# Kernel optimization log

Measured on AMD Instinct MI355X. Metric: run time of the kernel, lower is better.

## Reference

```python
import jax, jax.numpy as jnp
import numpy as np

B, T, D, H, FF_MULT, WINDOW = 4, 2048, 256, 8, 4, 64
HD = D // H
FF = FF_MULT * D
EPS = 1e-5


def _layer_norm(x, g, b):
    m = jnp.mean(x, axis=-1, keepdims=True)
    v = jnp.mean(jnp.square(x - m), axis=-1, keepdims=True)
    return (x - m) / jnp.sqrt(v + EPS) * g + b


def setup_inputs() -> dict:
    key = jax.random.key(0)
    ks = jax.random.split(key, 6)
    scale = 0.02
    return {
        "x": jax.random.normal(ks[0], (B, T, D), jnp.float32),
        "ln1_g": jnp.ones((D,), jnp.float32),
        "ln1_b": jnp.zeros((D,), jnp.float32),
        "in_proj_w": jax.random.normal(ks[1], (D, 3 * D), jnp.float32) * scale,
        "in_proj_b": jnp.zeros((3 * D,), jnp.float32),
        "out_w": jax.random.normal(ks[2], (D, D), jnp.float32) * scale,
        "out_b": jnp.zeros((D,), jnp.float32),
        "ln2_g": jnp.ones((D,), jnp.float32),
        "ln2_b": jnp.zeros((D,), jnp.float32),
        "w1": jax.random.normal(ks[3], (D, FF), jnp.float32) * scale,
        "b1": jnp.zeros((FF,), jnp.float32),
        "w2": jax.random.normal(ks[4], (FF, D), jnp.float32) * scale,
        "b2": jnp.zeros((D,), jnp.float32),
        "window": WINDOW,
    }


def reference(x, ln1_g, ln1_b, in_proj_w, in_proj_b, out_w, out_b,
              ln2_g, ln2_b, w1, b1, w2, b2, window):
    Bv, Tv, Dv = x.shape
    xn = _layer_norm(x, ln1_g, ln1_b)                      # norm1(x) used as q,k,v
    qkv = xn @ in_proj_w + in_proj_b                       # [B,T,3D]
    q, k, v = jnp.split(qkv, 3, axis=-1)

    def to_heads(t):
        return t.reshape(Bv, Tv, H, HD).transpose(0, 2, 1, 3)  # [B,H,T,HD]

    q, k, v = to_heads(q), to_heads(k), to_heads(v)
    scores = jnp.einsum('bhqd,bhkd->bhqk', q, k) / jnp.sqrt(jnp.float32(HD))
    i = jnp.arange(Tv)[:, None]
    j = jnp.arange(Tv)[None, :]
    band = jnp.abs(j - i) <= window                        # True = allowed
    scores = jnp.where(band, scores, -jnp.inf)
    attn = jax.nn.softmax(scores, axis=-1)
    o = jnp.einsum('bhqk,bhkd->bhqd', attn, v)
    o = o.transpose(0, 2, 1, 3).reshape(Bv, Tv, Dv)
    h_out = o @ out_w + out_b                              # attn output
    y = x + h_out
    ff = _layer_norm(y, ln2_g, ln2_b)
    ff = jax.nn.gelu(ff @ w1 + b1, approximate=False) @ w2 + b2
    return x + ff                                          # note: residual from x, not y
```

## Files before the change

kernel.cpp:

```cpp
#include <hip/hip_runtime.h>
#include <math.h>

#define T_SEQ 2048

typedef float  fx4 __attribute__((ext_vector_type(4)));
typedef short  sx4 __attribute__((ext_vector_type(4)));
typedef short  sx8 __attribute__((ext_vector_type(8)));
typedef unsigned short u16;

static __device__ __forceinline__ u16 f2b(float f) {
  unsigned u = __builtin_bit_cast(unsigned, f);
  u += 0x7fffu + ((u >> 16) & 1u);
  return (u16)(u >> 16);
}
static __device__ __forceinline__ float b2f(u16 v) {
  unsigned u = ((unsigned)v) << 16;
  return __builtin_bit_cast(float, u);
}

static __device__ __forceinline__ fx4 mfma16(sx4 a, sx4 b, fx4 c) {
  return __builtin_amdgcn_mfma_f32_16x16x16bf16_1k(a, b, c, 0, 0, 0);
}
static __device__ __forceinline__ fx4 mfma32(sx8 a, sx8 b, fx4 c) {
  return __builtin_amdgcn_mfma_f32_16x16x32_bf16(a, b, c, 0, 0, 0);
}

static __device__ __forceinline__ void gload16(const void* g, void* l) {
  __builtin_amdgcn_global_load_lds(
      (const __attribute__((address_space(1))) unsigned*)g,
      (__attribute__((address_space(3))) unsigned*)l, 16, 0, 0);
}

__global__ __launch_bounds__(256) void prep_k(
    const float* __restrict__ x, const float* __restrict__ g1,
    const float* __restrict__ b1, u16* __restrict__ xn, u16* __restrict__ xb,
    const float* __restrict__ ipw, const float* __restrict__ outw,
    const float* __restrict__ w1, const float* __restrict__ w2,
    u16* __restrict__ ipwT, u16* __restrict__ outwT,
    u16* __restrict__ w1T, u16* __restrict__ w2T) {
  const int bid = blockIdx.x;
  if (bid < 2048) {
    const int row = bid * 4 + (threadIdx.x >> 6);
    const int l = threadIdx.x & 63;
    fx4 v = *(const fx4*)&x[(size_t)row * 256 + l * 4];
    float s = v.x + v.y + v.z + v.w;
    float q = v.x * v.x + v.y * v.y + v.z * v.z + v.w * v.w;
#pragma unroll
    for (int off = 1; off < 64; off <<= 1) {
      s += __shfl_xor(s, off);
      q += __shfl_xor(q, off);
    }
    const float mean = s * (1.0f / 256.0f);
    const float var = q * (1.0f / 256.0f) - mean * mean;
    const float rstd = rsqrtf(var + 1e-5f);
    fx4 gv = *(const fx4*)&g1[l * 4];
    fx4 bv = *(const fx4*)&b1[l * 4];
    sx4 o, xo;
    o[0] = (short)f2b((v.x - mean) * rstd * gv.x + bv.x);
    o[1] = (short)f2b((v.y - mean) * rstd * gv.y + bv.y);
    o[2] = (short)f2b((v.z - mean) * rstd * gv.z + bv.z);
    o[3] = (short)f2b((v.w - mean) * rstd * gv.w + bv.w);
    xo[0] = (short)f2b(v.x);
    xo[1] = (short)f2b(v.y);
    xo[2] = (short)f2b(v.z);
    xo[3] = (short)f2b(v.w);
    *(sx4*)&xn[(size_t)row * 256 + l * 4] = o;
    *(sx4*)&xb[(size_t)row * 256 + l * 4] = xo;
    return;
  }
  const int tb = bid - 2048;
  const float* in; u16* out; int K, N, loc;
  if (tb < 192)      { in = ipw;  out = ipwT;  K = 256;  N = 768;  loc = tb; }
  else if (tb < 256) { in = outw; out = outwT; K = 256;  N = 256;  loc = tb - 192; }
  else if (tb < 512) { in = w1;   out = w1T;   K = 256;  N = 1024; loc = tb - 256; }
  else               { in = w2;   out = w2T;   K = 1024; N = 256;  loc = tb - 512; }
  const int ntx = N >> 5;
  const int by = (loc / ntx) << 5;
  const int bx = (loc % ntx) << 5;
  __shared__ float t[32][33];
  const int c = threadIdx.x & 31, r0 = threadIdx.x >> 5;
#pragma unroll
  for (int i = 0; i < 4; ++i)
    t[r0 + i * 8][c] = in[(size_t)(by + r0 + i * 8) * N + bx + c];
  __syncthreads();
#pragma unroll
  for (int i = 0; i < 4; ++i) {
    const int r = r0 + i * 8;
    out[(size_t)(bx + r) * K + by + c] = f2b(t[c][r]);
  }
}

template <int BM, int BN, int KD, int ND, int OP, int NGRP>
__global__ __launch_bounds__(256) void gemm3_k(const u16* __restrict__ A,
                                               const u16* __restrict__ Wt,
                                               const float* __restrict__ bias,
                                               const float* __restrict__ resid,
                                               void* __restrict__ outp) {
  constexpr int BK = 64;
  constexpr int WM = BM / 2, WN = BN / 2;
  constexpr int FM = WM / 16, FN = WN / 16;
  constexpr int NT = KD / BK;
  __shared__ __align__(16) char smem[(2 * BM + 2 * BN) * BK * 2];
  auto As = (u16(*)[BM][BK])smem;
  auto Bs = (u16(*)[BN][BK])(smem + 2 * BM * BK * 2);
  const int tid = threadIdx.x;
  const int id = blockIdx.x;
  const int bm = ((id & 7) + 8 * ((id >> 3) / NGRP)) * BM;
  const int bn = ((id >> 3) % NGRP) * BN;
  const int l = tid & 63, wid = tid >> 6;
  const int wm = wid >> 1, wn = wid & 1;
  const int lq = l & 15, lg = l >> 4;

  auto stage = [&](int buf, int k0) {
#pragma unroll
    for (int i = 0; i < (BM * BK) / 2048; ++i) {
      const int row = (tid >> 3) + 32 * i;
      const int c = (tid & 7) ^ (row & 7);
      gload16(&A[(size_t)(bm + row) * KD + k0 + c * 8], &As[buf][row][(tid & 7) * 8]);
    }
#pragma unroll
    for (int i = 0; i < (BN * BK) / 2048; ++i) {
      const int row = (tid >> 3) + 32 * i;
      const int c = (tid & 7) ^ (row & 7);
      gload16(&Wt[(size_t)(bn + row) * KD + k0 + c * 8], &Bs[buf][row][(tid & 7) * 8]);
    }
  };

  fx4 acc[FM][FN] = {};
  stage(0, 0);
  int cur = 0;
  for (int t = 0; t < NT; ++t) {
    __syncthreads();
    if (t + 1 < NT) stage(cur ^ 1, (t + 1) * BK);
#pragma unroll
    for (int kk = 0; kk < BK; kk += 32) {
      sx8 aF[FM], bF[FN];
#pragma unroll
      for (int m = 0; m < FM; ++m) {
        const int row = wm * WM + m * 16 + lq;
        const int c = ((kk >> 3) + lg) ^ (row & 7);
        aF[m] = *(const sx8*)&As[cur][row][c * 8];
      }
#pragma unroll
      for (int n = 0; n < FN; ++n) {
        const int row = wn * WN + n * 16 + lq;
        const int c = ((kk >> 3) + lg) ^ (row & 7);
        bF[n] = *(const sx8*)&Bs[cur][row][c * 8];
      }
#pragma unroll
      for (int m = 0; m < FM; ++m)
#pragma unroll
        for (int n = 0; n < FN; ++n) acc[m][n] = mfma32(aF[m], bF[n], acc[m][n]);
    }
    cur ^= 1;
  }

  __syncthreads();
  if (OP == 1) {
    auto C = (float(*)[BN + 8])smem;
#pragma unroll
    for (int m = 0; m < FM; ++m)
#pragma unroll
      for (int n = 0; n < FN; ++n) {
        const int col = wn * WN + n * 16 + lq;
        const float bv = bias[bn + col];
#pragma unroll
        for (int r = 0; r < 4; ++r)
          C[wm * WM + m * 16 + lg * 4 + r][col] = acc[m][n][r] + bv;
      }
    __syncthreads();
    constexpr int CH = (BM * BN / 4) / 256;
#pragma unroll
    for (int i = 0; i < CH; ++i) {
      const int t = tid + i * 256;
      const int row = t / (BN / 4), c = t % (BN / 4);
      fx4 v = *(const fx4*)&C[row][c * 4];
      const fx4 rr = *(const fx4*)&resid[(size_t)(bm + row) * ND + bn + c * 4];
      v += rr;
      *(fx4*)&((float*)outp)[(size_t)(bm + row) * ND + bn + c * 4] = v;
    }
  } else {
    auto C = (u16(*)[BN + 8])smem;
#pragma unroll
    for (int m = 0; m < FM; ++m)
#pragma unroll
      for (int n = 0; n < FN; ++n) {
        const int col = wn * WN + n * 16 + lq;
        const float bv = bias[bn + col];
#pragma unroll
        for (int r = 0; r < 4; ++r) {
          float v = acc[m][n][r] + bv;
          if (OP == 2) v = 0.5f * v * (1.0f + erff(v * 0.70710678118654752f));
          C[wm * WM + m * 16 + lg * 4 + r][col] = f2b(v);
        }
      }
    __syncthreads();
    constexpr int CH = (BM * BN / 8) / 256;
#pragma unroll
    for (int i = 0; i < CH; ++i) {
      const int t = tid + i * 256;
      const int row = t / (BN / 8), c = t % (BN / 8);
      *(sx8*)&((u16*)outp)[(size_t)(bm + row) * ND + bn + c * 8] = *(const sx8*)&C[row][c * 8];
    }
  }
}

__global__ __launch_bounds__(256) void gemmln_k(const u16* __restrict__ A,
                                                const u16* __restrict__ Wt,
                                                const float* __restrict__ bias,
                                                const u16* __restrict__ xb,
                                                const float* __restrict__ g,
                                                const float* __restrict__ bv2,
                                                u16* __restrict__ yn) {
  __shared__ __align__(16) char smem[18944];
  auto As = (u16(*)[32])smem;
  auto Bs = (u16(*)[32])(smem + 2048);
  auto red = (float(*)[2][2])(smem + 18432);
  auto Ys = (u16(*)[264])smem;
  const int tid = threadIdx.x;
  const int bm = blockIdx.x * 32;
  const int l = tid & 63, wid = tid >> 6;
  const int wm = wid >> 1, wn = wid & 1;
  const int lq = l & 15, lg = l >> 4;
  const int sr = tid >> 2, sc = (tid & 3) << 3;
  fx4 acc[8] = {};
  for (int k0 = 0; k0 < 256; k0 += 32) {
    if (tid < 128) gload16(&A[(size_t)(bm + (tid >> 2)) * 256 + k0 + ((tid & 3) << 3)],
                           &As[tid >> 2][(tid & 3) << 3]);
#pragma unroll
    for (int i = 0; i < 4; ++i)
      gload16(&Wt[(size_t)(sr + i * 64) * 256 + k0 + sc], &Bs[sr + i * 64][sc]);
    __syncthreads();
    const sx8 aF = *(const sx8*)&As[wm * 16 + lq][8 * lg];
#pragma unroll
    for (int n = 0; n < 8; ++n) {
      const sx8 bF = *(const sx8*)&Bs[wn * 128 + n * 16 + lq][8 * lg];
      acc[n] = mfma32(aF, bF, acc[n]);
    }
    __syncthreads();
  }
  float vv[8][4];
  float s[4] = {}, q[4] = {};
#pragma unroll
  for (int n = 0; n < 8; ++n) {
    const int col = wn * 128 + n * 16 + lq;
    const float bb = bias[col];
#pragma unroll
    for (int r = 0; r < 4; ++r) {
      const int row = bm + wm * 16 + lg * 4 + r;
      const float v = acc[n][r] + bb + b2f(xb[(size_t)row * 256 + col]);
      vv[n][r] = v;
      s[r] += v;
      q[r] += v * v;
    }
  }
#pragma unroll
  for (int off = 1; off < 16; off <<= 1) {
#pragma unroll
    for (int r = 0; r < 4; ++r) {
      s[r] += __shfl_xor(s[r], off);
      q[r] += __shfl_xor(q[r], off);
    }
  }
  if (lq == 0) {
#pragma unroll
    for (int r = 0; r < 4; ++r) {
      red[wm * 16 + lg * 4 + r][wn][0] = s[r];
      red[wm * 16 + lg * 4 + r][wn][1] = q[r];
    }
  }
  __syncthreads();
  float mean4[4], rs4[4];
#pragma unroll
  for (int r = 0; r < 4; ++r) {
    const int rr = wm * 16 + lg * 4 + r;
    const float st = red[rr][0][0] + red[rr][1][0];
    const float qt = red[rr][0][1] + red[rr][1][1];
    mean4[r] = st * (1.0f / 256.0f);
    const float var = qt * (1.0f / 256.0f) - mean4[r] * mean4[r];
    rs4[r] = rsqrtf(var + 1e-5f);
  }
  __syncthreads();
#pragma unroll
  for (int n = 0; n < 8; ++n) {
    const int col = wn * 128 + n * 16 + lq;
    const float gc = g[col], bc = bv2[col];
#pragma unroll
    for (int r = 0; r < 4; ++r)
      Ys[wm * 16 + lg * 4 + r][col] = f2b((vv[n][r] - mean4[r]) * rs4[r] * gc + bc);
  }
  __syncthreads();
#pragma unroll
  for (int i = 0; i < 4; ++i) {
    const int t = tid + i * 256;
    const int row = t >> 5, c = t & 31;
    *(sx8*)&yn[(size_t)(bm + row) * 256 + c * 8] = *(const sx8*)&Ys[row][c * 8];
  }
}

__global__ __launch_bounds__(512) void attn_k(const u16* __restrict__ qkv,
                                              u16* __restrict__ o) {
  __shared__ u16 Qs[128][32];
  __shared__ u16 Ks[256][32];
  __shared__ u16 Vs[32][264];
  const int blk = blockIdx.x;
  const int tile = blk & 15;
  const int bh = blk >> 4;
  const int h = bh & 7;
  const int b = bh >> 3;
  const int q0 = tile << 7;
  const int kstart = max(0, q0 - 64);
  const int kend = min(T_SEQ, q0 + 192);
  const int nk = kend - kstart;
  const int tid = threadIdx.x;
  const float scale = 0.17677669529663687f;

  {
    const int r = tid >> 2, c8 = (tid & 3) << 3;
    gload16(&qkv[(size_t)(b * T_SEQ + q0 + r) * 768 + h * 32 + c8], &Qs[r][c8]);
  }
  for (int r0 = 0; r0 < nk; r0 += 128) {
    const int r = r0 + (tid >> 2);
    if (r < nk) {
      const int c8 = (tid & 3) << 3;
      gload16(&qkv[(size_t)(b * T_SEQ + kstart + r) * 768 + 256 + h * 32 + c8], &Ks[r][c8]);
    }
  }
  for (int e = tid * 4; e < nk * 32; e += 2048) {
    const int r = e >> 5, c = e & 31;
    sx4 v = *(const sx4*)&qkv[(size_t)(b * T_SEQ + kstart + r) * 768 + 512 + h * 32 + c];
    Vs[c + 0][r] = v[0];
    Vs[c + 1][r] = v[1];
    Vs[c + 2][r] = v[2];
    Vs[c + 3][r] = v[3];
  }
  __syncthreads();

  const int w = tid >> 6, l = tid & 63;
  const int lq = l & 15, lg = l >> 4;
  const int qw0 = q0 + w * 16;
  const int iq = qw0 + lq;
  const sx8 qB = *(const sx8*)&Qs[w * 16 + lq][8 * lg];
  float lsum = 0.0f;
  fx4 acc0 = {0.f, 0.f, 0.f, 0.f}, acc1 = {0.f, 0.f, 0.f, 0.f};
  const int rt0 = max(0, qw0 - 64 - kstart) >> 4;
  const int rt1 = (min(kend, qw0 + 80) - kstart) >> 4;
  for (int rt = rt0; rt < rt1; ++rt) {
    const int kb = kstart + (rt << 4);
    const sx8 kA = *(const sx8*)&Ks[(rt << 4) + lq][8 * lg];
    fx4 zero = {0.f, 0.f, 0.f, 0.f};
    fx4 sc = mfma32(kA, qB, zero);
    sx4 pB;
#pragma unroll
    for (int r = 0; r < 4; ++r) {
      const int dd = kb + 4 * lg + r - iq;
      const float sv = (dd >= -64 && dd <= 64) ? fminf(sc[r] * scale, 30.0f) : -100.0f;
      const float p = __expf(sv);
      lsum += p;
      pB[r] = (short)f2b(p);
    }
    const sx4 vA0 = *(const sx4*)&Vs[lq][(rt << 4) + 4 * lg];
    const sx4 vA1 = *(const sx4*)&Vs[16 + lq][(rt << 4) + 4 * lg];
    acc0 = mfma16(vA0, pB, acc0);
    acc1 = mfma16(vA1, pB, acc1);
  }
  lsum += __shfl_xor(lsum, 16);
  lsum += __shfl_xor(lsum, 32);
  const float rl = 1.0f / lsum;

  __syncthreads();
  auto Os = (u16(*)[32])Qs;
#pragma unroll
  for (int r = 0; r < 4; ++r) {
    Os[w * 16 + lq][4 * lg + r] = f2b(acc0[r] * rl);
    Os[w * 16 + lq][16 + 4 * lg + r] = f2b(acc1[r] * rl);
  }
  __syncthreads();
  {
    const int row = tid >> 2, c = tid & 3;
    *(sx8*)&o[(size_t)(b * T_SEQ + q0 + row) * 256 + h * 32 + c * 8] =
        *(const sx8*)&Os[row][c * 8];
  }
}

extern "C" void kernel_launch(void* const* d_in, const int* in_sizes, int n_in,
                              void* d_out, int out_size, void* d_ws, size_t ws_size,
                              hipStream_t stream) {
  const float* x    = (const float*)d_in[0];
  const float* ln1g = (const float*)d_in[1];
  const float* ln1b = (const float*)d_in[2];
  const float* ipw  = (const float*)d_in[3];
  const float* ipb  = (const float*)d_in[4];
  const float* outw = (const float*)d_in[5];
  const float* outb = (const float*)d_in[6];
  const float* ln2g = (const float*)d_in[7];
  const float* ln2b = (const float*)d_in[8];
  const float* w1   = (const float*)d_in[9];
  const float* b1   = (const float*)d_in[10];
  const float* w2   = (const float*)d_in[11];
  const float* b2   = (const float*)d_in[12];

  char* ws = (char*)d_ws;
  u16*   xn   = (u16*)(ws);
  u16*   qkvb = (u16*)(ws + (4ull << 20));
  u16*   o    = (u16*)(ws + (16ull << 20));
  u16*   yn   = (u16*)(ws + (20ull << 20));
  u16*   hh   = (u16*)(ws + (24ull << 20));
  u16*   xb   = (u16*)(ws + (40ull << 20));
  u16*   ipwT = (u16*)(ws + (44ull << 20));
  u16*   outwT= (u16*)(ws + (44ull << 20) + (512ull << 10));
  u16*   w1T  = (u16*)(ws + (45ull << 20));
  u16*   w2T  = (u16*)(ws + (45ull << 20) + (512ull << 10));

  prep_k<<<2816, 256, 0, stream>>>(x, ln1g, ln1b, xn, xb, ipw, outw, w1, w2,
                                   ipwT, outwT, w1T, w2T);
  gemm3_k<128, 128, 256, 768, 0, 6><<<384, 256, 0, stream>>>(xn, ipwT, ipb, nullptr, qkvb);
  attn_k<<<512, 512, 0, stream>>>(qkvb, o);
  gemmln_k<<<256, 256, 0, stream>>>(o, outwT, outb, xb, ln2g, ln2b, yn);
  gemm3_k<128, 128, 256, 1024, 2, 8><<<512, 256, 0, stream>>>(yn, w1T, b1, nullptr, hh);
  gemm3_k<64, 128, 1024, 256, 1, 2><<<256, 256, 0, stream>>>(hh, w2T, b2, x, (float*)d_out);
}
```

Baseline: 62.68 us.

## Fuse both MLP GEMMs and GELU into one kernel keeping hidden in LDS

Replaces the two MLP GEMM launches (FC1+GELU writing the hidden activation to global memory, then FC2+residual) with a single kernel. Each block owns 32 rows, loops over 64-wide hidden chunks, computes FC1+GELU into shared memory and accumulates FC2 directly, double-buffering the weight chunks. This removes the global round trip of the 8192x1024 hidden tensor and one launch. In exchange it uses only 256 blocks with about 148KB of shared memory each (one block per CU), adds more barriers per chunk, and every block re-reads all of W1 and W2.

Result: slower. 70.54 us (+12.5%).

```diff
diff --git a/kernel.cpp b/kernel.cpp
--- a/kernel.cpp
+++ b/kernel.cpp
@@ -156,8 +156,8 @@
   }
 
   __syncthreads();
-  if (OP == 1) {
-    auto C = (float(*)[BN + 8])smem;
+  {
+    auto C = (u16(*)[BN + 8])smem;
 #pragma unroll
     for (int m = 0; m < FM; ++m)
 #pragma unroll
@@ -165,32 +165,8 @@
         const int col = wn * WN + n * 16 + lq;
         const float bv = bias[bn + col];
 #pragma unroll
-        for (int r = 0; r < 4; ++r)
-          C[wm * WM + m * 16 + lg * 4 + r][col] = acc[m][n][r] + bv;
-      }
-    __syncthreads();
-    constexpr int CH = (BM * BN / 4) / 256;
-#pragma unroll
-    for (int i = 0; i < CH; ++i) {
-      const int t = tid + i * 256;
-      const int row = t / (BN / 4), c = t % (BN / 4);
-      fx4 v = *(const fx4*)&C[row][c * 4];
-      const fx4 rr = *(const fx4*)&resid[(size_t)(bm + row) * ND + bn + c * 4];
-      v += rr;
-      *(fx4*)&((float*)outp)[(size_t)(bm + row) * ND + bn + c * 4] = v;
-    }
-  } else {
-    auto C = (u16(*)[BN + 8])smem;
-#pragma unroll
-    for (int m = 0; m < FM; ++m)
-#pragma unroll
-      for (int n = 0; n < FN; ++n) {
-        const int col = wn * WN + n * 16 + lq;
-        const float bv = bias[bn + col];
-#pragma unroll
         for (int r = 0; r < 4; ++r) {
           float v = acc[m][n][r] + bv;
-          if (OP == 2) v = 0.5f * v * (1.0f + erff(v * 0.70710678118654752f));
           C[wm * WM + m * 16 + lg * 4 + r][col] = f2b(v);
         }
       }
@@ -383,6 +359,124 @@
   }
 }
 
+__global__ __launch_bounds__(256) void mlp_k(const u16* __restrict__ yn,
+                                             const u16* __restrict__ w1T,
+                                             const u16* __restrict__ w2T,
+                                             const float* __restrict__ b1,
+                                             const float* __restrict__ b2,
+                                             const float* __restrict__ x,
+                                             float* __restrict__ out) {
+  __shared__ __align__(16) char smem[151552];
+  auto As = (u16(*)[32][64])smem;
+  auto Hs = (u16(*)[64])(smem + 16384);
+  const int tid = threadIdx.x;
+  const int bm = blockIdx.x * 32;
+  const int l = tid & 63, wid = tid >> 6;
+  const int lq = l & 15, lg = l >> 4;
+
+#pragma unroll
+  for (int s = 0; s < 4; ++s) {
+    const int row = tid >> 3, ch = tid & 7;
+    gload16(&yn[(size_t)(bm + row) * 256 + s * 64 + ((ch ^ (row & 7)) << 3)],
+            &As[s][row][ch << 3]);
+  }
+  auto stage_w = [&](int b, int c) {
+    auto W1 = (u16(*)[64][64])(smem + 20480 + b * 32768);
+    auto W2 = (u16(*)[64])(smem + 86016 + b * 32768);
+#pragma unroll
+    for (int j = 0; j < 8; ++j) {
+      const int p = tid + j * 256;
+      const int s = p >> 9, w = p & 511, row = w >> 3, ch = w & 7;
+      gload16(&w1T[(size_t)(c * 64 + row) * 256 + s * 64 + ((ch ^ (row & 7)) << 3)],
+              &W1[s][row][ch << 3]);
+    }
+#pragma unroll
+    for (int j = 0; j < 8; ++j) {
+      const int p = tid + j * 256;
+      const int row = p >> 3, ch = p & 7;
+      gload16(&w2T[(size_t)row * 1024 + c * 64 + ((ch ^ (row & 7)) << 3)],
+              &W2[row][ch << 3]);
+    }
+  };
+
+  fx4 acc[2][4] = {};
+  stage_w(0, 0);
+  __syncthreads();
+  int cur = 0;
+  for (int c = 0; c < 16; ++c) {
+    if (c) __syncthreads();
+    if (c + 1 < 16) stage_w(cur ^ 1, c + 1);
+    auto W1 = (u16(*)[64][64])(smem + 20480 + cur * 32768);
+    auto W2 = (u16(*)[64])(smem + 86016 + cur * 32768);
+    const int rfw = wid * 16 + lq;
+    fx4 hacc0 = {0.f, 0.f, 0.f, 0.f}, hacc1 = {0.f, 0.f, 0.f, 0.f};
+#pragma unroll
+    for (int s = 0; s < 4; ++s)
+#pragma unroll
+      for (int kk = 0; kk < 2; ++kk) {
+        const int cc = kk * 4 + lg;
+        const sx8 bF = *(const sx8*)&W1[s][rfw][(cc ^ (rfw & 7)) << 3];
+        const sx8 aF0 = *(const sx8*)&As[s][lq][(cc ^ (lq & 7)) << 3];
+        const sx8 aF1 = *(const sx8*)&As[s][16 + lq][(cc ^ (lq & 7)) << 3];
+        hacc0 = mfma32(aF0, bF, hacc0);
+        hacc1 = mfma32(aF1, bF, hacc1);
+      }
+    const float bb1 = b1[c * 64 + rfw];
+#pragma unroll
+    for (int r = 0; r < 4; ++r) {
+      {
+        float v = hacc0[r] + bb1;
+        v = 0.5f * v * (1.0f + erff(v * 0.70710678118654752f));
+        const int row = 4 * lg + r;
+        Hs[row][(((rfw >> 3) ^ (row & 7)) << 3) | (rfw & 7)] = f2b(v);
+      }
+      {
+        float v = hacc1[r] + bb1;
+        v = 0.5f * v * (1.0f + erff(v * 0.70710678118654752f));
+        const int row = 16 + 4 * lg + r;
+        Hs[row][(((rfw >> 3) ^ (row & 7)) << 3) | (rfw & 7)] = f2b(v);
+      }
+    }
+    asm volatile("s_waitcnt lgkmcnt(0)\n\ts_barrier" ::: "memory");
+#pragma unroll
+    for (int kk = 0; kk < 2; ++kk) {
+      const int cc = kk * 4 + lg;
+      const sx8 aH0 = *(const sx8*)&Hs[lq][(cc ^ (lq & 7)) << 3];
+      const sx8 aH1 = *(const sx8*)&Hs[16 + lq][(cc ^ (lq & 7)) << 3];
+#pragma unroll
+      for (int n = 0; n < 4; ++n) {
+        const int rw = wid * 64 + n * 16 + lq;
+        const sx8 bW = *(const sx8*)&W2[rw][(cc ^ (rw & 7)) << 3];
+        acc[0][n] = mfma32(aH0, bW, acc[0][n]);
+        acc[1][n] = mfma32(aH1, bW, acc[1][n]);
+      }
+    }
+    cur ^= 1;
+  }
+
+  __syncthreads();
+  auto Cs = (float(*)[264])smem;
+#pragma unroll
+  for (int n = 0; n < 4; ++n) {
+    const int col = wid * 64 + n * 16 + lq;
+    const float bb = b2[col];
+#pragma unroll
+    for (int m = 0; m < 2; ++m)
+#pragma unroll
+      for (int r = 0; r < 4; ++r)
+        Cs[m * 16 + 4 * lg + r][col] = acc[m][n][r] + bb;
+  }
+  __syncthreads();
+#pragma unroll
+  for (int j = 0; j < 8; ++j) {
+    const int p = tid + j * 256;
+    const int row = p >> 6, c4 = (p & 63) << 2;
+    fx4 v = *(const fx4*)&Cs[row][c4];
+    v += *(const fx4*)&x[(size_t)(bm + row) * 256 + c4];
+    *(fx4*)&out[(size_t)(bm + row) * 256 + c4] = v;
+  }
+}
+
 extern "C" void kernel_launch(void* const* d_in, const int* in_sizes, int n_in,
                               void* d_out, int out_size, void* d_ws, size_t ws_size,
                               hipStream_t stream) {
@@ -405,18 +499,16 @@
   u16*   qkvb = (u16*)(ws + (4ull << 20));
   u16*   o    = (u16*)(ws + (16ull << 20));
   u16*   yn   = (u16*)(ws + (20ull << 20));
-  u16*   hh   = (u16*)(ws + (24ull << 20));
-  u16*   xb   = (u16*)(ws + (40ull << 20));
-  u16*   ipwT = (u16*)(ws + (44ull << 20));
-  u16*   outwT= (u16*)(ws + (44ull << 20) + (512ull << 10));
-  u16*   w1T  = (u16*)(ws + (45ull << 20));
-  u16*   w2T  = (u16*)(ws + (45ull << 20) + (512ull << 10));
+  u16*   xb   = (u16*)(ws + (24ull << 20));
+  u16*   ipwT = (u16*)(ws + (28ull << 20));
+  u16*   outwT= (u16*)(ws + (28ull << 20) + (512ull << 10));
+  u16*   w1T  = (u16*)(ws + (29ull << 20));
+  u16*   w2T  = (u16*)(ws + (29ull << 20) + (512ull << 10));
 
   prep_k<<<2816, 256, 0, stream>>>(x, ln1g, ln1b, xn, xb, ipw, outw, w1, w2,
                                    ipwT, outwT, w1T, w2T);
   gemm3_k<128, 128, 256, 768, 0, 6><<<384, 256, 0, stream>>>(xn, ipwT, ipb, nullptr, qkvb);
   attn_k<<<512, 512, 0, stream>>>(qkvb, o);
   gemmln_k<<<256, 256, 0, stream>>>(o, outwT, outb, xb, ln2g, ln2b, yn);
-  gemm3_k<128, 128, 256, 1024, 2, 8><<<512, 256, 0, stream>>>(yn, w1T, b1, nullptr, hh);
-  gemm3_k<64, 128, 1024, 256, 1, 2><<<256, 256, 0, stream>>>(hh, w2T, b2, x, (float*)d_out);
-}
+  mlp_k<<<256, 256, 0, stream>>>(yn, w1T, w2T, b1, b2, x, (float*)d_out);
+}
```

## Use 8-wave blocks for GEMMs and double-buffer the out-proj+LN GEMM

Applied to the files above, without the earlier changes.

Doubles the threads per block in all GEMM kernels from 256 to 512, arranging waves in a 2x4 grid so each wave owns a smaller output tile. This adds latency hiding per block and shrinks per-wave accumulator registers. The out-projection plus LayerNorm kernel is reworked to use 64-wide K steps with double-buffered swizzled LDS staging, replacing its single-buffered loop with two barriers per step. In exchange it uses much more shared memory per block (about 73 KB), which may limit how many blocks fit on a CU, and it gives each wave fewer MFMAs per LDS load.

After: 59.15 us. 1.06x faster.

```diff
diff --git a/kernel.cpp b/kernel.cpp
--- a/kernel.cpp
+++ b/kernel.cpp
@@ -91,14 +91,14 @@
 }
 
 template <int BM, int BN, int KD, int ND, int OP, int NGRP>
-__global__ __launch_bounds__(256) void gemm3_k(const u16* __restrict__ A,
+__global__ __launch_bounds__(512) void gemm5_k(const u16* __restrict__ A,
                                                const u16* __restrict__ Wt,
                                                const float* __restrict__ bias,
                                                const float* __restrict__ resid,
                                                void* __restrict__ outp) {
   constexpr int BK = 64;
-  constexpr int WM = BM / 2, WN = BN / 2;
-  constexpr int FM = WM / 16, FN = WN / 16;
+  constexpr int WTM = BM / 2, WTN = BN / 4;
+  constexpr int FM = WTM / 16, FN = WTN / 16;
   constexpr int NT = KD / BK;
   __shared__ __align__(16) char smem[(2 * BM + 2 * BN) * BK * 2];
   auto As = (u16(*)[BM][BK])smem;
@@ -108,21 +108,23 @@
   const int bm = ((id & 7) + 8 * ((id >> 3) / NGRP)) * BM;
   const int bn = ((id >> 3) % NGRP) * BN;
   const int l = tid & 63, wid = tid >> 6;
-  const int wm = wid >> 1, wn = wid & 1;
+  const int wr = wid >> 2, wc = wid & 3;
   const int lq = l & 15, lg = l >> 4;
 
   auto stage = [&](int buf, int k0) {
 #pragma unroll
-    for (int i = 0; i < (BM * BK) / 2048; ++i) {
-      const int row = (tid >> 3) + 32 * i;
-      const int c = (tid & 7) ^ (row & 7);
-      gload16(&A[(size_t)(bm + row) * KD + k0 + c * 8], &As[buf][row][(tid & 7) * 8]);
-    }
-#pragma unroll
-    for (int i = 0; i < (BN * BK) / 2048; ++i) {
-      const int row = (tid >> 3) + 32 * i;
-      const int c = (tid & 7) ^ (row & 7);
-      gload16(&Wt[(size_t)(bn + row) * KD + k0 + c * 8], &Bs[buf][row][(tid & 7) * 8]);
+    for (int i = 0; i < BM / 64; ++i) {
+      const int p = tid + i * 512;
+      const int row = p >> 3, ch = p & 7;
+      gload16(&A[(size_t)(bm + row) * KD + k0 + ((ch ^ (row & 7)) << 3)],
+              &As[buf][row][ch << 3]);
+    }
+#pragma unroll
+    for (int i = 0; i < BN / 64; ++i) {
+      const int p = tid + i * 512;
+      const int row = p >> 3, ch = p & 7;
+      gload16(&Wt[(size_t)(bn + row) * KD + k0 + ((ch ^ (row & 7)) << 3)],
+              &Bs[buf][row][ch << 3]);
     }
   };
 
@@ -137,15 +139,13 @@
       sx8 aF[FM], bF[FN];
 #pragma unroll
       for (int m = 0; m < FM; ++m) {
-        const int row = wm * WM + m * 16 + lq;
-        const int c = ((kk >> 3) + lg) ^ (row & 7);
-        aF[m] = *(const sx8*)&As[cur][row][c * 8];
+        const int row = wr * WTM + m * 16 + lq;
+        aF[m] = *(const sx8*)&As[cur][row][((((kk >> 3) + lg) ^ (row & 7)) << 3)];
       }
 #pragma unroll
       for (int n = 0; n < FN; ++n) {
-        const int row = wn * WN + n * 16 + lq;
-        const int c = ((kk >> 3) + lg) ^ (row & 7);
-        bF[n] = *(const sx8*)&Bs[cur][row][c * 8];
+        const int row = wc * WTN + n * 16 + lq;
+        bF[n] = *(const sx8*)&Bs[cur][row][((((kk >> 3) + lg) ^ (row & 7)) << 3)];
       }
 #pragma unroll
       for (int m = 0; m < FM; ++m)
@@ -162,21 +162,20 @@
     for (int m = 0; m < FM; ++m)
 #pragma unroll
       for (int n = 0; n < FN; ++n) {
-        const int col = wn * WN + n * 16 + lq;
+        const int col = wc * WTN + n * 16 + lq;
         const float bv = bias[bn + col];
 #pragma unroll
         for (int r = 0; r < 4; ++r)
-          C[wm * WM + m * 16 + lg * 4 + r][col] = acc[m][n][r] + bv;
+          C[wr * WTM + m * 16 + lg * 4 + r][col] = acc[m][n][r] + bv;
       }
     __syncthreads();
-    constexpr int CH = (BM * BN / 4) / 256;
+    constexpr int CH = (BM * BN / 4) / 512;
 #pragma unroll
     for (int i = 0; i < CH; ++i) {
-      const int t = tid + i * 256;
+      const int t = tid + i * 512;
       const int row = t / (BN / 4), c = t % (BN / 4);
       fx4 v = *(const fx4*)&C[row][c * 4];
-      const fx4 rr = *(const fx4*)&resid[(size_t)(bm + row) * ND + bn + c * 4];
-      v += rr;
+      v += *(const fx4*)&resid[(size_t)(bm + row) * ND + bn + c * 4];
       *(fx4*)&((float*)outp)[(size_t)(bm + row) * ND + bn + c * 4] = v;
     }
   } else {
@@ -185,69 +184,88 @@
     for (int m = 0; m < FM; ++m)
 #pragma unroll
       for (int n = 0; n < FN; ++n) {
-        const int col = wn * WN + n * 16 + lq;
+        const int col = wc * WTN + n * 16 + lq;
         const float bv = bias[bn + col];
 #pragma unroll
         for (int r = 0; r < 4; ++r) {
           float v = acc[m][n][r] + bv;
           if (OP == 2) v = 0.5f * v * (1.0f + erff(v * 0.70710678118654752f));
-          C[wm * WM + m * 16 + lg * 4 + r][col] = f2b(v);
+          C[wr * WTM + m * 16 + lg * 4 + r][col] = f2b(v);
         }
       }
     __syncthreads();
-    constexpr int CH = (BM * BN / 8) / 256;
+    constexpr int CH = (BM * BN / 8) / 512;
 #pragma unroll
     for (int i = 0; i < CH; ++i) {
-      const int t = tid + i * 256;
+      const int t = tid + i * 512;
       const int row = t / (BN / 8), c = t % (BN / 8);
       *(sx8*)&((u16*)outp)[(size_t)(bm + row) * ND + bn + c * 8] = *(const sx8*)&C[row][c * 8];
     }
   }
 }
 
-__global__ __launch_bounds__(256) void gemmln_k(const u16* __restrict__ A,
+__global__ __launch_bounds__(512) void gemmln_k(const u16* __restrict__ A,
                                                 const u16* __restrict__ Wt,
                                                 const float* __restrict__ bias,
                                                 const u16* __restrict__ xb,
                                                 const float* __restrict__ g,
                                                 const float* __restrict__ bv2,
                                                 u16* __restrict__ yn) {
-  __shared__ __align__(16) char smem[18944];
-  auto As = (u16(*)[32])smem;
-  auto Bs = (u16(*)[32])(smem + 2048);
-  auto red = (float(*)[2][2])(smem + 18432);
+  __shared__ __align__(16) char smem[74752];
+  auto As = (u16(*)[32][64])smem;
+  auto Bs = (u16(*)[256][64])(smem + 8192);
+  auto red = (float(*)[4][2])(smem + 73728);
   auto Ys = (u16(*)[264])smem;
   const int tid = threadIdx.x;
   const int bm = blockIdx.x * 32;
   const int l = tid & 63, wid = tid >> 6;
-  const int wm = wid >> 1, wn = wid & 1;
+  const int wr = wid >> 2, wc = wid & 3;
   const int lq = l & 15, lg = l >> 4;
-  const int sr = tid >> 2, sc = (tid & 3) << 3;
-  fx4 acc[8] = {};
-  for (int k0 = 0; k0 < 256; k0 += 32) {
-    if (tid < 128) gload16(&A[(size_t)(bm + (tid >> 2)) * 256 + k0 + ((tid & 3) << 3)],
-                           &As[tid >> 2][(tid & 3) << 3]);
-#pragma unroll
-    for (int i = 0; i < 4; ++i)
-      gload16(&Wt[(size_t)(sr + i * 64) * 256 + k0 + sc], &Bs[sr + i * 64][sc]);
+
+  auto stage = [&](int buf, int k0) {
+    if (tid < 256) {
+      const int row = tid >> 3, ch = tid & 7;
+      gload16(&A[(size_t)(bm + row) * 256 + k0 + ((ch ^ (row & 7)) << 3)],
+              &As[buf][row][ch << 3]);
+    }
+#pragma unroll
+    for (int i = 0; i < 4; ++i) {
+      const int p = tid + i * 512;
+      const int row = p >> 3, ch = p & 7;
+      gload16(&Wt[(size_t)row * 256 + k0 + ((ch ^ (row & 7)) << 3)],
+              &Bs[buf][row][ch << 3]);
+    }
+  };
+
+  fx4 acc[4] = {};
+  stage(0, 0);
+  int cur = 0;
+  for (int t = 0; t < 4; ++t) {
     __syncthreads();
-    const sx8 aF = *(const sx8*)&As[wm * 16 + lq][8 * lg];
-#pragma unroll
-    for (int n = 0; n < 8; ++n) {
-      const sx8 bF = *(const sx8*)&Bs[wn * 128 + n * 16 + lq][8 * lg];
-      acc[n] = mfma32(aF, bF, acc[n]);
-    }
-    __syncthreads();
-  }
-  float vv[8][4];
+    if (t + 1 < 4) stage(cur ^ 1, (t + 1) * 64);
+#pragma unroll
+    for (int kk = 0; kk < 64; kk += 32) {
+      const int arow = wr * 16 + lq;
+      const sx8 aF = *(const sx8*)&As[cur][arow][((((kk >> 3) + lg) ^ (arow & 7)) << 3)];
+#pragma unroll
+      for (int n = 0; n < 4; ++n) {
+        const int brow = wc * 64 + n * 16 + lq;
+        const sx8 bF = *(const sx8*)&Bs[cur][brow][((((kk >> 3) + lg) ^ (brow & 7)) << 3)];
+        acc[n] = mfma32(aF, bF, acc[n]);
+      }
+    }
+    cur ^= 1;
+  }
+
+  float vv[4][4];
   float s[4] = {}, q[4] = {};
 #pragma unroll
-  for (int n = 0; n < 8; ++n) {
-    const int col = wn * 128 + n * 16 + lq;
+  for (int n = 0; n < 4; ++n) {
+    const int col = wc * 64 + n * 16 + lq;
     const float bb = bias[col];
 #pragma unroll
     for (int r = 0; r < 4; ++r) {
-      const int row = bm + wm * 16 + lg * 4 + r;
+      const int row = bm + wr * 16 + lg * 4 + r;
       const float v = acc[n][r] + bb + b2f(xb[(size_t)row * 256 + col]);
       vv[n][r] = v;
       s[r] += v;
@@ -262,37 +280,38 @@
       q[r] += __shfl_xor(q[r], off);
     }
   }
+  __syncthreads();
   if (lq == 0) {
 #pragma unroll
     for (int r = 0; r < 4; ++r) {
-      red[wm * 16 + lg * 4 + r][wn][0] = s[r];
-      red[wm * 16 + lg * 4 + r][wn][1] = q[r];
+      red[wr * 16 + lg * 4 + r][wc][0] = s[r];
+      red[wr * 16 + lg * 4 + r][wc][1] = q[r];
     }
   }
   __syncthreads();
   float mean4[4], rs4[4];
 #pragma unroll
   for (int r = 0; r < 4; ++r) {
-    const int rr = wm * 16 + lg * 4 + r;
-    const float st = red[rr][0][0] + red[rr][1][0];
-    const float qt = red[rr][0][1] + red[rr][1][1];
+    const int rr = wr * 16 + lg * 4 + r;
+    const float st = red[rr][0][0] + red[rr][1][0] + red[rr][2][0] + red[rr][3][0];
+    const float qt = red[rr][0][1] + red[rr][1][1] + red[rr][2][1] + red[rr][3][1];
     mean4[r] = st * (1.0f / 256.0f);
     const float var = qt * (1.0f / 256.0f) - mean4[r] * mean4[r];
     rs4[r] = rsqrtf(var + 1e-5f);
   }
   __syncthreads();
 #pragma unroll
-  for (int n = 0; n < 8; ++n) {
-    const int col = wn * 128 + n * 16 + lq;
+  for (int n = 0; n < 4; ++n) {
+    const int col = wc * 64 + n * 16 + lq;
     const float gc = g[col], bc = bv2[col];
 #pragma unroll
     for (int r = 0; r < 4; ++r)
-      Ys[wm * 16 + lg * 4 + r][col] = f2b((vv[n][r] - mean4[r]) * rs4[r] * gc + bc);
-  }
-  __syncthreads();
-#pragma unroll
-  for (int i = 0; i < 4; ++i) {
-    const int t = tid + i * 256;
+      Ys[wr * 16 + lg * 4 + r][col] = f2b((vv[n][r] - mean4[r]) * rs4[r] * gc + bc);
+  }
+  __syncthreads();
+#pragma unroll
+  for (int i = 0; i < 2; ++i) {
+    const int t = tid + i * 512;
     const int row = t >> 5, c = t & 31;
     *(sx8*)&yn[(size_t)(bm + row) * 256 + c * 8] = *(const sx8*)&Ys[row][c * 8];
   }
@@ -414,9 +433,9 @@
 
   prep_k<<<2816, 256, 0, stream>>>(x, ln1g, ln1b, xn, xb, ipw, outw, w1, w2,
                                    ipwT, outwT, w1T, w2T);
-  gemm3_k<128, 128, 256, 768, 0, 6><<<384, 256, 0, stream>>>(xn, ipwT, ipb, nullptr, qkvb);
+  gemm5_k<128, 128, 256, 768, 0, 6><<<384, 512, 0, stream>>>(xn, ipwT, ipb, nullptr, qkvb);
   attn_k<<<512, 512, 0, stream>>>(qkvb, o);
-  gemmln_k<<<256, 256, 0, stream>>>(o, outwT, outb, xb, ln2g, ln2b, yn);
-  gemm3_k<128, 128, 256, 1024, 2, 8><<<512, 256, 0, stream>>>(yn, w1T, b1, nullptr, hh);
-  gemm3_k<64, 128, 1024, 256, 1, 2><<<256, 256, 0, stream>>>(hh, w2T, b2, x, (float*)d_out);
-}
+  gemmln_k<<<256, 512, 0, stream>>>(o, outwT, outb, xb, ln2g, ln2b, yn);
+  gemm5_k<128, 128, 256, 1024, 2, 8><<<512, 512, 0, stream>>>(yn, w1T, b1, nullptr, hh);
+  gemm5_k<64, 128, 1024, 256, 1, 2><<<256, 512, 0, stream>>>(hh, w2T, b2, x, (float*)d_out);
+}
```
